# Optimization experiments

Measured on AMD Instinct MI355X. Metric: run time of the kernel, lower is better.

The kernel has to match this reference:

```python
import jax, jax.numpy as jnp
import numpy as np

D_MODEL = 1280
D_BOTTLE = 64
LN_EPS = 1e-5


def setup_inputs() -> dict:
    key = jax.random.key(0)
    k1, k2, k3, k4, k5 = jax.random.split(key, 5)
    x = jax.random.normal(k1, (16, 1500, D_MODEL), dtype=jnp.float32)
    # LayerNorm params (torch default: weight=1, bias=0; use random-ish gamma for a stronger test)
    gamma = jnp.ones((D_MODEL,), dtype=jnp.float32)
    beta = jnp.zeros((D_MODEL,), dtype=jnp.float32)
    # Linear weights stored torch-style: [out, in]
    w_down = jax.random.normal(k2, (D_BOTTLE, D_MODEL), dtype=jnp.float32) * (1.0 / np.sqrt(D_MODEL))
    b_down = jax.random.normal(k3, (D_BOTTLE,), dtype=jnp.float32) * 0.01
    # up_proj is zero-initialized in the module; use small random values so gradients/outputs are nontrivial
    w_up = jax.random.normal(k4, (D_MODEL, D_BOTTLE), dtype=jnp.float32) * 0.01
    b_up = jax.random.normal(k5, (D_MODEL,), dtype=jnp.float32) * 0.01
    return {"x": x, "gamma": gamma, "beta": beta, "w_down": w_down, "b_down": b_down, "w_up": w_up, "b_up": b_up}


def reference(x, gamma, beta, w_down, b_down, w_up, b_up):
    # LayerNorm over last dim
    mean = jnp.mean(x, axis=-1, keepdims=True)
    var = jnp.mean(jnp.square(x - mean), axis=-1, keepdims=True)
    h = (x - mean) * jax.lax.rsqrt(var + LN_EPS) * gamma + beta
    # down-proj -> GELU -> up-proj (torch GELU default = exact erf form)
    h = jnp.einsum('bsd,kd->bsk', h, w_down) + b_down   # [B,S,64]
    h = jax.nn.gelu(h, approximate=False)
    h = jnp.einsum('bsk,dk->bsd', h, w_up) + b_up       # [B,S,1280]
    return h + x
```

## Files before the change

kernel.cpp:

```cpp
#include <hip/hip_runtime.h>
#include <hip/hip_bf16.h>

#define D_MODEL  1280
#define D_BOTTLE 64
#define LN_EPS   1e-5f
#define TM       16
#define GP       72

typedef __attribute__((ext_vector_type(8))) short short8;
typedef __attribute__((ext_vector_type(4))) float floatx4;

static __device__ inline unsigned short f2bf(float f) {
    __hip_bfloat16 h = __float2bfloat16(f);
    return *reinterpret_cast<unsigned short*>(&h);
}
static __device__ inline float bf2f(unsigned short u) {
    unsigned int v = ((unsigned int)u) << 16;
    return __uint_as_float(v);
}

__global__ void prep_weights(const float* __restrict__ wd, const float* __restrict__ gamma,
                             const float* __restrict__ wu,
                             unsigned short* __restrict__ wg, unsigned short* __restrict__ wu_b) {
    int i = blockIdx.x * blockDim.x + threadIdx.x;
    if (i < D_MODEL * D_BOTTLE) {
        int k = i % D_MODEL;
        wg[i]   = f2bf(wd[i] * gamma[k]);
        wu_b[i] = f2bf(wu[i]);
    }
}

__global__ void prep_reduce(const unsigned short* __restrict__ wg, const float* __restrict__ wd,
                            const float* __restrict__ beta, const float* __restrict__ b_down,
                            float* __restrict__ colsum, float* __restrict__ bd2) {
    const int n = blockIdx.x;
    const int t = threadIdx.x;
    float cs = 0.f, bb = 0.f;
    for (int k = t; k < D_MODEL; k += 256) {
        cs += bf2f(wg[n * D_MODEL + k]);
        bb += wd[n * D_MODEL + k] * beta[k];
    }
    #pragma unroll
    for (int m = 1; m < 64; m <<= 1) {
        cs += __shfl_xor(cs, m);
        bb += __shfl_xor(bb, m);
    }
    __shared__ float scs[4], sbb[4];
    if ((t & 63) == 0) { scs[t >> 6] = cs; sbb[t >> 6] = bb; }
    __syncthreads();
    if (t == 0) {
        colsum[n] = scs[0] + scs[1] + scs[2] + scs[3];
        bd2[n]    = b_down[n] + sbb[0] + sbb[1] + sbb[2] + sbb[3];
    }
}

__global__ __launch_bounds__(256, 4) void adapter_kernel(
    const float* __restrict__ x,
    const unsigned short* __restrict__ wg, const float* __restrict__ colsum,
    const float* __restrict__ bd2,
    const unsigned short* __restrict__ wu_b, const float* __restrict__ b_up,
    float* __restrict__ out)
{
    __shared__ float s_mean[TM];
    __shared__ float s_rinv[TM];
    __shared__ unsigned short g_lds[TM * GP];

    const int tid  = threadIdx.x;
    const int wave = tid >> 6;
    const int lane = tid & 63;
    const int r0   = blockIdx.x * TM;

    {
        const int rloc = wave * 4 + (lane >> 4);
        const int lr   = lane & 15;
        const float* xrow = x + (size_t)(r0 + rloc) * D_MODEL;
        float s = 0.f, sq = 0.f;
        #pragma unroll
        for (int t = 0; t < 20; ++t) {
            float4 v = *reinterpret_cast<const float4*>(xrow + (lr + 16 * t) * 4);
            s  += v.x + v.y + v.z + v.w;
            sq += v.x * v.x + v.y * v.y + v.z * v.z + v.w * v.w;
        }
        #pragma unroll
        for (int m = 1; m < 16; m <<= 1) {
            s  += __shfl_xor(s, m);
            sq += __shfl_xor(sq, m);
        }
        const float mean = s * (1.f / D_MODEL);
        const float var  = sq * (1.f / D_MODEL) - mean * mean;
        if (lr == 0) {
            s_mean[rloc] = mean;
            s_rinv[rloc] = rsqrtf(var + LN_EPS);
        }
    }
    __syncthreads();

    const int l15   = lane & 15;
    const int khalf = lane >> 4;
    const int n0    = wave * 16;
    const int nn    = n0 + l15;

    floatx4 acc = {0.f, 0.f, 0.f, 0.f};
    {
        const float* arow = x + (size_t)(r0 + l15) * D_MODEL + khalf * 8;
        const unsigned short* brow = wg + (size_t)nn * D_MODEL + khalf * 8;
        #pragma unroll 4
        for (int kk = 0; kk < 40; ++kk) {
            float4 a0 = *reinterpret_cast<const float4*>(arow + kk * 32);
            float4 a1 = *reinterpret_cast<const float4*>(arow + kk * 32 + 4);
            short8 a;
            a[0] = (short)f2bf(a0.x); a[1] = (short)f2bf(a0.y);
            a[2] = (short)f2bf(a0.z); a[3] = (short)f2bf(a0.w);
            a[4] = (short)f2bf(a1.x); a[5] = (short)f2bf(a1.y);
            a[6] = (short)f2bf(a1.z); a[7] = (short)f2bf(a1.w);
            short8 b = *reinterpret_cast<const short8*>(brow + kk * 32);
            acc = __builtin_amdgcn_mfma_f32_16x16x32_bf16(a, b, acc, 0, 0, 0);
        }
    }

    {
        const float cs  = colsum[nn];
        const float bdn = bd2[nn];
        #pragma unroll
        for (int r = 0; r < 4; ++r) {
            const int m = khalf * 4 + r;
            const float yv = s_rinv[m] * (acc[r] - s_mean[m] * cs) + bdn;
            const float gv = 0.5f * yv * (1.f + erff(yv * 0.70710678118654752f));
            g_lds[m * GP + nn] = f2bf(gv);
        }
    }
    __syncthreads();

    short8 ga0 = *reinterpret_cast<const short8*>(g_lds + l15 * GP +  0 + khalf * 8);
    short8 ga1 = *reinterpret_cast<const short8*>(g_lds + l15 * GP + 32 + khalf * 8);

    const int m_base = khalf * 4;
    #pragma unroll 4
    for (int i = 0; i < 20; ++i) {
        const int d0 = (i * 4 + wave) * 16;
        const int d  = d0 + l15;
        const unsigned short* bptr = wu_b + (size_t)d * D_BOTTLE + khalf * 8;
        short8 b0 = *reinterpret_cast<const short8*>(bptr);
        short8 b1 = *reinterpret_cast<const short8*>(bptr + 32);
        floatx4 acc2 = {0.f, 0.f, 0.f, 0.f};
        acc2 = __builtin_amdgcn_mfma_f32_16x16x32_bf16(ga0, b0, acc2, 0, 0, 0);
        acc2 = __builtin_amdgcn_mfma_f32_16x16x32_bf16(ga1, b1, acc2, 0, 0, 0);
        const float bu = b_up[d];
        #pragma unroll
        for (int r = 0; r < 4; ++r) {
            const size_t idx = (size_t)(r0 + m_base + r) * D_MODEL + d;
            out[idx] = acc2[r] + bu + x[idx];
        }
    }
}

extern "C" void kernel_launch(void* const* d_in, const int* in_sizes, int n_in,
                              void* d_out, int out_size, void* d_ws, size_t ws_size,
                              hipStream_t stream) {
    const float* x      = (const float*)d_in[0];
    const float* gamma  = (const float*)d_in[1];
    const float* beta   = (const float*)d_in[2];
    const float* w_down = (const float*)d_in[3];
    const float* b_down = (const float*)d_in[4];
    const float* w_up   = (const float*)d_in[5];
    const float* b_up   = (const float*)d_in[6];
    float* out = (float*)d_out;

    unsigned short* wg   = (unsigned short*)d_ws;
    unsigned short* wu_b = wg + D_MODEL * D_BOTTLE;
    float* colsum = (float*)(wu_b + D_MODEL * D_BOTTLE);
    float* bd2    = colsum + D_BOTTLE;

    prep_weights<<<(D_MODEL * D_BOTTLE + 255) / 256, 256, 0, stream>>>(w_down, gamma, w_up, wg, wu_b);
    prep_reduce<<<D_BOTTLE, 256, 0, stream>>>(wg, w_down, beta, b_down, colsum, bd2);

    const int rows = in_sizes[0] / D_MODEL;
    adapter_kernel<<<rows / TM, 256, 0, stream>>>(x, wg, colsum, bd2, wu_b, b_up, out);
}
```

Before: 331.4 us.

## Stage x rows once in LDS as bf16 and reuse for GEMM and residual

Each block now loads its x rows from global memory once, computes the LayerNorm statistics from registers, and writes a swizzled bf16 copy to LDS. Both the down-projection MFMA operand and the residual add read from that copy, so x is no longer fetched three times from global memory. The row tile shrinks from 16 to 8 so the larger LDS footprint still fits, and the occupancy hint rises to 6. In exchange, half of each 16-row MFMA tile does wasted work, and the residual now adds a bf16-rounded x instead of the fp32 value, which costs output accuracy.

```diff
diff --git a/kernel.cpp b/kernel.cpp
--- a/kernel.cpp
+++ b/kernel.cpp
@@ -4,7 +4,8 @@
 #define D_MODEL  1280
 #define D_BOTTLE 64
 #define LN_EPS   1e-5f
-#define TM       16
+#define TM       8
+#define ROWB     2560
 #define GP       72
 
 typedef __attribute__((ext_vector_type(8))) short short8;
@@ -54,16 +55,16 @@
     }
 }
 
-__global__ __launch_bounds__(256, 4) void adapter_kernel(
+__global__ __launch_bounds__(256, 6) void adapter_kernel(
     const float* __restrict__ x,
     const unsigned short* __restrict__ wg, const float* __restrict__ colsum,
     const float* __restrict__ bd2,
     const unsigned short* __restrict__ wu_b, const float* __restrict__ b_up,
     float* __restrict__ out)
 {
-    __shared__ float s_mean[TM];
-    __shared__ float s_rinv[TM];
+    __shared__ unsigned char  h_raw[TM * ROWB];
     __shared__ unsigned short g_lds[TM * GP];
+    __shared__ float s_mean[TM], s_rinv[TM];
 
     const int tid  = threadIdx.x;
     const int wave = tid >> 6;
@@ -71,48 +72,56 @@
     const int r0   = blockIdx.x * TM;
 
     {
-        const int rloc = wave * 4 + (lane >> 4);
-        const int lr   = lane & 15;
+        const int rloc = tid >> 5;
+        const int li   = tid & 31;
         const float* xrow = x + (size_t)(r0 + rloc) * D_MODEL;
+        float4 v0 = *reinterpret_cast<const float4*>(xrow + li * 4 +    0);
+        float4 v1 = *reinterpret_cast<const float4*>(xrow + li * 4 +  128);
+        float4 v2 = *reinterpret_cast<const float4*>(xrow + li * 4 +  256);
+        float4 v3 = *reinterpret_cast<const float4*>(xrow + li * 4 +  384);
+        float4 v4 = *reinterpret_cast<const float4*>(xrow + li * 4 +  512);
+        float4 v5 = *reinterpret_cast<const float4*>(xrow + li * 4 +  640);
+        float4 v6 = *reinterpret_cast<const float4*>(xrow + li * 4 +  768);
+        float4 v7 = *reinterpret_cast<const float4*>(xrow + li * 4 +  896);
+        float4 v8 = *reinterpret_cast<const float4*>(xrow + li * 4 + 1024);
+        float4 v9 = *reinterpret_cast<const float4*>(xrow + li * 4 + 1152);
+
         float s = 0.f, sq = 0.f;
+        #define ACC4(v) { s += v.x + v.y + v.z + v.w; sq += v.x*v.x + v.y*v.y + v.z*v.z + v.w*v.w; }
+        ACC4(v0) ACC4(v1) ACC4(v2) ACC4(v3) ACC4(v4)
+        ACC4(v5) ACC4(v6) ACC4(v7) ACC4(v8) ACC4(v9)
+        #undef ACC4
         #pragma unroll
-        for (int t = 0; t < 20; ++t) {
-            float4 v = *reinterpret_cast<const float4*>(xrow + (lr + 16 * t) * 4);
-            s  += v.x + v.y + v.z + v.w;
-            sq += v.x * v.x + v.y * v.y + v.z * v.z + v.w * v.w;
-        }
-        #pragma unroll
-        for (int m = 1; m < 16; m <<= 1) {
+        for (int m = 1; m < 32; m <<= 1) {
             s  += __shfl_xor(s, m);
             sq += __shfl_xor(sq, m);
         }
         const float mean = s * (1.f / D_MODEL);
         const float var  = sq * (1.f / D_MODEL) - mean * mean;
-        if (lr == 0) {
-            s_mean[rloc] = mean;
-            s_rinv[rloc] = rsqrtf(var + LN_EPS);
-        }
+        if (li == 0) { s_mean[rloc] = mean; s_rinv[rloc] = rsqrtf(var + LN_EPS); }
+
+        const int swz = rloc << 4;
+        #define ST4(v, t) { ushort4 pk; pk.x = f2bf(v.x); pk.y = f2bf(v.y); pk.z = f2bf(v.z); pk.w = f2bf(v.w); \
+            *reinterpret_cast<ushort4*>(h_raw + rloc * ROWB + ((li * 8 + 256 * (t)) ^ swz)) = pk; }
+        ST4(v0,0) ST4(v1,1) ST4(v2,2) ST4(v3,3) ST4(v4,4)
+        ST4(v5,5) ST4(v6,6) ST4(v7,7) ST4(v8,8) ST4(v9,9)
+        #undef ST4
     }
     __syncthreads();
 
     const int l15   = lane & 15;
     const int khalf = lane >> 4;
-    const int n0    = wave * 16;
-    const int nn    = n0 + l15;
+    const int lr    = l15 & 7;
+    const int nn    = wave * 16 + l15;
 
     floatx4 acc = {0.f, 0.f, 0.f, 0.f};
     {
-        const float* arow = x + (size_t)(r0 + l15) * D_MODEL + khalf * 8;
         const unsigned short* brow = wg + (size_t)nn * D_MODEL + khalf * 8;
+        const unsigned char*  abase = h_raw + lr * ROWB;
+        const int aswz = lr << 4;
         #pragma unroll 4
         for (int kk = 0; kk < 40; ++kk) {
-            float4 a0 = *reinterpret_cast<const float4*>(arow + kk * 32);
-            float4 a1 = *reinterpret_cast<const float4*>(arow + kk * 32 + 4);
-            short8 a;
-            a[0] = (short)f2bf(a0.x); a[1] = (short)f2bf(a0.y);
-            a[2] = (short)f2bf(a0.z); a[3] = (short)f2bf(a0.w);
-            a[4] = (short)f2bf(a1.x); a[5] = (short)f2bf(a1.y);
-            a[6] = (short)f2bf(a1.z); a[7] = (short)f2bf(a1.w);
+            short8 a = *reinterpret_cast<const short8*>(abase + ((kk * 64 + khalf * 16) ^ aswz));
             short8 b = *reinterpret_cast<const short8*>(brow + kk * 32);
             acc = __builtin_amdgcn_mfma_f32_16x16x32_bf16(a, b, acc, 0, 0, 0);
         }
@@ -121,24 +130,24 @@
     {
         const float cs  = colsum[nn];
         const float bdn = bd2[nn];
-        #pragma unroll
-        for (int r = 0; r < 4; ++r) {
-            const int m = khalf * 4 + r;
-            const float yv = s_rinv[m] * (acc[r] - s_mean[m] * cs) + bdn;
-            const float gv = 0.5f * yv * (1.f + erff(yv * 0.70710678118654752f));
-            g_lds[m * GP + nn] = f2bf(gv);
+        if (khalf < 2) {
+            #pragma unroll
+            for (int r = 0; r < 4; ++r) {
+                const int m = khalf * 4 + r;
+                const float yv = s_rinv[m] * (acc[r] - s_mean[m] * cs) + bdn;
+                const float gv = 0.5f * yv * (1.f + erff(yv * 0.70710678118654752f));
+                g_lds[m * GP + nn] = f2bf(gv);
+            }
         }
     }
     __syncthreads();
 
-    short8 ga0 = *reinterpret_cast<const short8*>(g_lds + l15 * GP +  0 + khalf * 8);
-    short8 ga1 = *reinterpret_cast<const short8*>(g_lds + l15 * GP + 32 + khalf * 8);
+    short8 ga0 = *reinterpret_cast<const short8*>(g_lds + lr * GP +  0 + khalf * 8);
+    short8 ga1 = *reinterpret_cast<const short8*>(g_lds + lr * GP + 32 + khalf * 8);
 
-    const int m_base = khalf * 4;
-    #pragma unroll 4
+    #pragma unroll 2
     for (int i = 0; i < 20; ++i) {
-        const int d0 = (i * 4 + wave) * 16;
-        const int d  = d0 + l15;
+        const int d = (i * 4 + wave) * 16 + l15;
         const unsigned short* bptr = wu_b + (size_t)d * D_BOTTLE + khalf * 8;
         short8 b0 = *reinterpret_cast<const short8*>(bptr);
         short8 b1 = *reinterpret_cast<const short8*>(bptr + 32);
@@ -146,10 +155,14 @@
         acc2 = __builtin_amdgcn_mfma_f32_16x16x32_bf16(ga0, b0, acc2, 0, 0, 0);
         acc2 = __builtin_amdgcn_mfma_f32_16x16x32_bf16(ga1, b1, acc2, 0, 0, 0);
         const float bu = b_up[d];
-        #pragma unroll
-        for (int r = 0; r < 4; ++r) {
-            const size_t idx = (size_t)(r0 + m_base + r) * D_MODEL + d;
-            out[idx] = acc2[r] + bu + x[idx];
+        if (khalf < 2) {
+            #pragma unroll
+            for (int r = 0; r < 4; ++r) {
+                const int m = khalf * 4 + r;
+                const unsigned short xr16 =
+                    *reinterpret_cast<const unsigned short*>(h_raw + m * ROWB + ((d * 2) ^ (m << 4)));
+                out[(size_t)(r0 + m) * D_MODEL + d] = acc2[r] + bu + bf2f(xr16);
+            }
         }
     }
 }
```

Result: faster. 317.5 us (-4.2%).
